# Performance work log

Hardware: AMD Instinct MI355X
Metric: run time of the kernel (lower is better)

## Reference

```python
import jax, jax.numpy as jnp
import numpy as np

B, L, DIM = 1, 2048, 4096
H, KV, HD = 32, 8, 128
REP = H // KV
SCALE = HD ** -0.5
ROPE_BASE = 10000.0


def rope_traditional(x, offset=0):
    # x: [B, H, L, D] ; traditional RoPE rotates interleaved pairs (x[2i], x[2i+1])
    D = x.shape[-1]
    Lx = x.shape[2]
    pos = jnp.arange(offset, offset + Lx, dtype=jnp.float32)            # [L]
    inv_freq = ROPE_BASE ** (-jnp.arange(0, D, 2, dtype=jnp.float32) / D)  # [D/2]
    ang = pos[:, None] * inv_freq[None, :]                               # [L, D/2]
    c, s = jnp.cos(ang), jnp.sin(ang)
    x1 = x[..., 0::2]
    x2 = x[..., 1::2]
    r1 = x1 * c - x2 * s
    r2 = x1 * s + x2 * c
    return jnp.stack([r1, r2], axis=-1).reshape(x.shape).astype(x.dtype)


def setup_inputs() -> dict:
    key = jax.random.key(0)
    k0, k1, k2, k3, k4 = jax.random.split(key, 5)
    x = jax.random.normal(k0, (B, L, DIM), dtype=jnp.float32)
    wq = jax.random.normal(k1, (DIM, H * HD), dtype=jnp.float32) * 0.02
    wk = jax.random.normal(k2, (DIM, KV * HD), dtype=jnp.float32) * 0.02
    wv = jax.random.normal(k3, (DIM, KV * HD), dtype=jnp.float32) * 0.02
    wo = jax.random.normal(k4, (H * HD, DIM), dtype=jnp.float32) * 0.02
    # additive causal mask (prefill)
    causal = jnp.tril(jnp.ones((L, L), dtype=bool))
    mask = jnp.where(causal, 0.0, -1e9).astype(jnp.float32)
    return {"x": x, "wq": wq, "wk": wk, "wv": wv, "wo": wo, "mask": mask}


def reference(x, wq, wk, wv, wo, mask):
    Bx, Lx, _ = x.shape
    q = (x @ wq).reshape(Bx, Lx, H, HD).transpose(0, 2, 1, 3)   # [B,H,L,hd]
    k = (x @ wk).reshape(Bx, Lx, KV, HD).transpose(0, 2, 1, 3)  # [B,KV,L,hd]
    v = (x @ wv).reshape(Bx, Lx, KV, HD).transpose(0, 2, 1, 3)
    # GQA head repeat (each kv head repeated REP times contiguously)
    k = jnp.repeat(k, REP, axis=1)  # [B,H,L,hd]
    v = jnp.repeat(v, REP, axis=1)
    # RoPE applied after repeat (cache=None branch), offset 0
    q = rope_traditional(q)
    k = rope_traditional(k)
    scores = jnp.einsum("bhld,bhmd->bhlm", q * SCALE, k) + mask  # [B,H,L,L]
    probs = jax.nn.softmax(scores.astype(jnp.float32), axis=-1).astype(scores.dtype)
    out = jnp.einsum("bhlm,bhmd->bhld", probs, v)
    out = out.transpose(0, 2, 1, 3).reshape(Bx, Lx, H * HD)
    return out @ wo, k, v
```

## Files before the change

### kernel.cpp

```cpp
#include <hip/hip_runtime.h>
#include <hip/hip_bf16.h>
#include <math.h>


#define L_SEQ 2048
#define DIM   4096
#define NH    32
#define NKV   8
#define HD    128
#define SCALE 0.08838834764831845f

typedef __bf16 bf16x8 __attribute__((ext_vector_type(8)));
typedef __bf16 bf16x4 __attribute__((ext_vector_type(4)));
typedef __bf16 bf16x2 __attribute__((ext_vector_type(2)));
typedef float  f32x4  __attribute__((ext_vector_type(4)));

__device__ __forceinline__ void gld16(const void* g, void* l) {
  __builtin_amdgcn_global_load_lds(
      (const __attribute__((address_space(1))) void*)g,
      (__attribute__((address_space(3))) void*)l, 16, 0, 0);
}

__global__ void cast_bf16_kernel(const float* __restrict__ in,
                                 __bf16* __restrict__ out, long n4) {
  long i = blockIdx.x * (long)blockDim.x + threadIdx.x;
  if (i >= n4) return;
  float4 f = reinterpret_cast<const float4*>(in)[i];
  bf16x4 o;
  o[0] = (__bf16)f.x; o[1] = (__bf16)f.y; o[2] = (__bf16)f.z; o[3] = (__bf16)f.w;
  reinterpret_cast<bf16x4*>(out)[i] = o;
}

__global__ void tcast_kernel(const float* __restrict__ in0, __bf16* __restrict__ out0,
                             const float* __restrict__ in1, __bf16* __restrict__ out1,
                             int K, int N) {
  __shared__ float tile[32][33];
  const float* in  = blockIdx.z ? in1  : in0;
  __bf16*     out  = blockIdx.z ? out1 : out0;
  int n0 = blockIdx.x * 32, k0 = blockIdx.y * 32;
  int tx = threadIdx.x & 31, ty = threadIdx.x >> 5;
#pragma unroll
  for (int i = 0; i < 4; ++i)
    tile[ty + i * 8][tx] = in[(long)(k0 + ty + i * 8) * N + n0 + tx];
  __syncthreads();
#pragma unroll
  for (int i = 0; i < 4; ++i)
    out[(long)(n0 + ty + i * 8) * K + k0 + tx] = (__bf16)tile[tx][ty + i * 8];
}

#define GBM 128
#define GBN 256
#define ABYTES  (GBM * 64 * 2)
#define BBYTES  (GBN * 64 * 2)
#define BUFBYTES (ABYTES + BBYTES)

__global__ __launch_bounds__(512, 2) void gemm256(
    const __bf16* __restrict__ A, const __bf16* __restrict__ B0,
    const __bf16* __restrict__ B1, void* __restrict__ C0, void* __restrict__ C1,
    int M, int N, int K, int mode) {
  __shared__ char lds[3 * BUFBYTES] __attribute__((aligned(16)));
  const __bf16* Bt = blockIdx.z ? B1 : B0;
  void* C = blockIdx.z ? C1 : C0;

  const int nwg = gridDim.x * gridDim.y;
  const int bid = blockIdx.y * gridDim.x + blockIdx.x;
  const int swz = (bid & 7) * (nwg >> 3) + (bid >> 3);
  const int n0 = (swz % gridDim.x) * GBN;
  const int m0 = (swz / gridDim.x) * GBM;

  const int t = threadIdx.x, wave = t >> 6, lane = t & 63;
  const int quad = lane >> 4, l16 = lane & 15;
  const int wm = (wave >> 2) * 64, wn = (wave & 3) * 64;

  const int srow = t >> 3;
  const int scol = ((t & 7) ^ (srow & 7)) * 8;
  const __bf16* pa = A  + (long)(m0 + srow) * K + scol;
  const __bf16* pb = Bt + (long)(n0 + srow) * K + scol;
  const long K64 = (long)64 * K;
  const int ldsA = wave * 1024;
  const int ldsB = ABYTES + wave * 1024;

  int aoff[2][4], boff[2][4];
#pragma unroll
  for (int ks = 0; ks < 2; ++ks) {
    const int sw = ((ks * 4 + quad) ^ (l16 & 7)) * 16;
#pragma unroll
    for (int i = 0; i < 4; ++i) {
      aoff[ks][i] = (wm + i * 16 + l16) * 128 + sw;
      boff[ks][i] = ABYTES + (wn + i * 16 + l16) * 128 + sw;
    }
  }

  f32x4 acc[4][4] = {};
  const int nt = K >> 6;

  {
    char* bb = lds;
#pragma unroll
    for (int pt = 0; pt < 2; ++pt) {
      gld16(pa,           bb + ldsA);
      gld16(pa + K64,     bb + ldsA + 8192);
      gld16(pb,           bb + ldsB);
      gld16(pb + K64,     bb + ldsB + 8192);
      gld16(pb + 2 * K64, bb + ldsB + 16384);
      gld16(pb + 3 * K64, bb + ldsB + 24576);
      pa += 64; pb += 64;
      bb += BUFBYTES;
    }
  }

  char* cb = lds;
  char* sb = lds + 2 * BUFBYTES;

#pragma unroll 1
  for (int kt = 0; kt < nt - 1; ++kt) {
    asm volatile("s_waitcnt vmcnt(6)" ::: "memory");
    __builtin_amdgcn_s_barrier();
    bf16x8 af[4], bfr[4];
#pragma unroll
    for (int i = 0; i < 4; ++i) {
      af[i]  = *(const bf16x8*)(cb + aoff[0][i]);
      bfr[i] = *(const bf16x8*)(cb + boff[0][i]);
    }
    if (kt + 2 < nt) {
      gld16(pa,           sb + ldsA);
      gld16(pa + K64,     sb + ldsA + 8192);
      gld16(pb,           sb + ldsB);
      gld16(pb + K64,     sb + ldsB + 8192);
      gld16(pb + 2 * K64, sb + ldsB + 16384);
      gld16(pb + 3 * K64, sb + ldsB + 24576);
      pa += 64; pb += 64;
    }
    __builtin_amdgcn_s_setprio(1);
#pragma unroll
    for (int tm = 0; tm < 4; ++tm)
#pragma unroll
      for (int tn = 0; tn < 4; ++tn)
        acc[tm][tn] = __builtin_amdgcn_mfma_f32_16x16x32_bf16(
            af[tm], bfr[tn], acc[tm][tn], 0, 0, 0);
    __builtin_amdgcn_s_setprio(0);
#pragma unroll
    for (int i = 0; i < 4; ++i) {
      af[i]  = *(const bf16x8*)(cb + aoff[1][i]);
      bfr[i] = *(const bf16x8*)(cb + boff[1][i]);
    }
    __builtin_amdgcn_s_setprio(1);
#pragma unroll
    for (int tm = 0; tm < 4; ++tm)
#pragma unroll
      for (int tn = 0; tn < 4; ++tn)
        acc[tm][tn] = __builtin_amdgcn_mfma_f32_16x16x32_bf16(
            af[tm], bfr[tn], acc[tm][tn], 0, 0, 0);
    __builtin_amdgcn_s_setprio(0);
    cb += BUFBYTES; if (cb == lds + 3 * BUFBYTES) cb = lds;
    sb += BUFBYTES; if (sb == lds + 3 * BUFBYTES) sb = lds;
  }

  asm volatile("s_waitcnt vmcnt(0)" ::: "memory");
  __builtin_amdgcn_s_barrier();
  {
    bf16x8 af[4], bfr[4];
#pragma unroll
    for (int ks = 0; ks < 2; ++ks) {
#pragma unroll
      for (int i = 0; i < 4; ++i) {
        af[i]  = *(const bf16x8*)(cb + aoff[ks][i]);
        bfr[i] = *(const bf16x8*)(cb + boff[ks][i]);
      }
      __builtin_amdgcn_s_setprio(1);
#pragma unroll
      for (int tm = 0; tm < 4; ++tm)
#pragma unroll
        for (int tn = 0; tn < 4; ++tn)
          acc[tm][tn] = __builtin_amdgcn_mfma_f32_16x16x32_bf16(
              af[tm], bfr[tn], acc[tm][tn], 0, 0, 0);
      __builtin_amdgcn_s_setprio(0);
    }
  }

#pragma unroll
  for (int tm = 0; tm < 4; ++tm)
#pragma unroll
    for (int tn = 0; tn < 4; ++tn)
#pragma unroll
      for (int r = 0; r < 4; ++r) {
        int row = m0 + wm + tm * 16 + quad * 4 + r;
        int col = n0 + wn + tn * 16 + l16;
        float v = acc[tm][tn][r];
        if (mode == 0) {
          ((float*)C)[(long)row * N + col] = v;
        } else {
          long idx = ((long)(col >> 7) * L_SEQ + row) * HD + (col & 127);
          ((__bf16*)C)[idx] = (__bf16)v;
        }
      }
}

#define NLOG2_10K 13.287712379549449f

__global__ void rope_q_kernel(__bf16* __restrict__ q ) {
  int idx = blockIdx.x * blockDim.x + threadIdx.x;
  int i = idx & 63, l = (idx >> 6) & 2047, h = idx >> 17;
  if (h >= NH) return;
  long base = ((long)h * L_SEQ + l) * HD + 2 * i;
  bf16x2 x12 = *(bf16x2*)(q + base);
  float x1 = (float)x12[0], x2 = (float)x12[1];
  float inv = exp2f((float)i * (-NLOG2_10K / 64.0f));
  float s, c; __sincosf((float)l * inv, &s, &c);
  bf16x2 o; o[0] = (__bf16)(x1 * c - x2 * s); o[1] = (__bf16)(x1 * s + x2 * c);
  *(bf16x2*)(q + base) = o;
}

__global__ void ropekv_kernel(__bf16* __restrict__ kb ,
                              const __bf16* __restrict__ vb,
                              float* __restrict__ kout ,
                              float* __restrict__ vout) {
  int idx = blockIdx.x * blockDim.x + threadIdx.x;
  int i = idx & 63, l = (idx >> 6) & 2047, kv = idx >> 17;
  if (kv >= NKV) return;
  long base = ((long)kv * L_SEQ + l) * HD + 2 * i;
  bf16x2 x12 = *(bf16x2*)(kb + base);
  float x1 = (float)x12[0], x2 = (float)x12[1];
  float inv = exp2f((float)i * (-NLOG2_10K / 64.0f));
  float s, c; __sincosf((float)l * inv, &s, &c);
  float r1 = x1 * c - x2 * s, r2 = x1 * s + x2 * c;
  bf16x2 o; o[0] = (__bf16)r1; o[1] = (__bf16)r2;
  *(bf16x2*)(kb + base) = o;
  float2 kf; kf.x = r1; kf.y = r2;
  bf16x2 vv = *(const bf16x2*)(vb + base);
  float2 vf; vf.x = (float)vv[0]; vf.y = (float)vv[1];
  long off = (long)(kv * 4) * L_SEQ * HD + (long)l * HD + 2 * i;
#pragma unroll
  for (int rr = 0; rr < 4; ++rr) {
    *(float2*)(kout + off) = kf;
    *(float2*)(vout + off) = vf;
    off += (long)L_SEQ * HD;
  }
}

__global__ void vtrans_kernel(const __bf16* __restrict__ Vh, __bf16* __restrict__ Vt) {
  __shared__ __bf16 tile[64 * 65];
  int kv = blockIdx.z, lb = blockIdx.x * 64, db = blockIdx.y * 64;
  int t = threadIdx.x;
#pragma unroll
  for (int it = 0; it < 2; ++it) {
    int c = it * 256 + t, r = c >> 3, pc = c & 7;
    bf16x8 v = *(const bf16x8*)(Vh + ((long)kv * L_SEQ + lb + r) * HD + db + pc * 8);
#pragma unroll
    for (int e = 0; e < 8; ++e) tile[r * 65 + pc * 8 + e] = v[e];
  }
  __syncthreads();
#pragma unroll
  for (int it = 0; it < 2; ++it) {
    int c = it * 256 + t, r = c >> 3, pc = c & 7;
    bf16x8 v;
#pragma unroll
    for (int e = 0; e < 8; ++e) v[e] = tile[(pc * 8 + e) * 65 + r];
    *(bf16x8*)(Vt + ((long)kv * HD + db + r) * L_SEQ + lb + pc * 8) = v;
  }
}

#define PSP 72
#define DTHR 8.0f

__global__ __launch_bounds__(256, 1) void attn4_kernel(
    const __bf16* __restrict__ Q, const __bf16* __restrict__ K,
    const __bf16* __restrict__ Vt, __bf16* __restrict__ O ) {
  __shared__ __bf16 Ks[2][64 * 128]  __attribute__((aligned(16)));
  __shared__ __bf16 Vts[2][128 * 64] __attribute__((aligned(16)));
  __shared__ __bf16 Ps[128 * PSP]    __attribute__((aligned(16)));

  const int b = blockIdx.x;
  const int kvg = b & 7;
  const int h   = kvg * 4 + ((b >> 3) & 3);
  const int qt  = 15 - (b >> 5);
  const int t = threadIdx.x, wave = t >> 6, lane = t & 63;
  const int quad = lane >> 4, l16 = lane & 15;
  const int mw = wave * 32;
  const __bf16* Kh = K  + (long)kvg * L_SEQ * HD;
  const __bf16* Vh = Vt + (long)kvg * HD * L_SEQ;
  const float SL2 = SCALE * 1.44269504f;

  int kr[4], kk[4], vr[4], vk[4];
#pragma unroll
  for (int it = 0; it < 4; ++it) {
    int c = it * 256 + t;
    kr[it] = c >> 4; kk[it] = ((c & 15) ^ (kr[it] & 7)) * 8;
    vr[it] = c >> 3; vk[it] = ((c & 7)  ^ (vr[it] & 7)) * 8;
  }

  const int nchunk = 2 * qt + 2;
  const int jdiag  = 2 * qt;

  int mq[2]; mq[0] = qt * 128 + mw + l16; mq[1] = mq[0] + 16;

  bf16x8 bq[2][4];
#pragma unroll
  for (int g = 0; g < 2; ++g) {
    const __bf16* qrow = Q + ((long)h * L_SEQ + mq[g]) * HD + quad * 8;
#pragma unroll
    for (int d = 0; d < 4; ++d) bq[g][d] = *(const bf16x8*)(qrow + d * 32);
  }

  f32x4 o_acc[2][8] = {};
  float m_run[2] = {-1e30f, -1e30f}, l_run[2] = {0.f, 0.f};

#pragma unroll
  for (int it = 0; it < 4; ++it) {
    gld16(Kh + (long)kr[it] * HD + kk[it],
          (char*)Ks[0] + (size_t)(it * 256 + wave * 64) * 16);
    gld16(Vh + (long)vr[it] * L_SEQ + vk[it],
          (char*)Vts[0] + (size_t)(it * 256 + wave * 64) * 16);
  }

#pragma unroll 1
  for (int j = 0; j < nchunk; ++j) {
    const int cur = j & 1;
    __syncthreads();
    if (j + 1 < nchunk) {
      const int nxt = cur ^ 1;
#pragma unroll
      for (int it = 0; it < 4; ++it) {
        gld16(Kh + (long)((j + 1) * 64 + kr[it]) * HD + kk[it],
              (char*)Ks[nxt] + (size_t)(it * 256 + wave * 64) * 16);
        gld16(Vh + (long)vr[it] * L_SEQ + (j + 1) * 64 + vk[it],
              (char*)Vts[nxt] + (size_t)(it * 256 + wave * 64) * 16);
      }
    }

    f32x4 s[2][4] = {};
#pragma unroll
    for (int dsi = 0; dsi < 4; ++dsi)
#pragma unroll
      for (int tn = 0; tn < 4; ++tn) {
        bf16x8 ak = *(const bf16x8*)((char*)Ks[cur] + (tn * 16 + l16) * 256 +
                                     (((dsi * 4 + quad) ^ (l16 & 7)) * 16));
        s[0][tn] = __builtin_amdgcn_mfma_f32_16x16x32_bf16(ak, bq[0][dsi], s[0][tn], 0, 0, 0);
        s[1][tn] = __builtin_amdgcn_mfma_f32_16x16x32_bf16(ak, bq[1][dsi], s[1][tn], 0, 0, 0);
      }

#pragma unroll
    for (int g = 0; g < 2; ++g) {
#pragma unroll
      for (int tn = 0; tn < 4; ++tn)
#pragma unroll
        for (int r = 0; r < 4; ++r) {
          float v = s[g][tn][r] * SL2;
          if (j >= jdiag && (j * 64 + tn * 16 + quad * 4 + r) > mq[g]) v = -3.0e38f;
          s[g][tn][r] = v;
        }
      float mx = -3.0e38f;
#pragma unroll
      for (int tn = 0; tn < 4; ++tn)
#pragma unroll
        for (int r = 0; r < 4; ++r) mx = fmaxf(mx, s[g][tn][r]);
      mx = fmaxf(mx, __shfl_xor(mx, 16, 64));
      mx = fmaxf(mx, __shfl_xor(mx, 32, 64));

      const bool defer = __all(mx - m_run[g] <= DTHR);
      const float mnew = defer ? m_run[g] : fmaxf(m_run[g], mx);

      float rs = 0.f;
#pragma unroll
      for (int tn = 0; tn < 4; ++tn)
#pragma unroll
        for (int r = 0; r < 4; ++r) {
          float pe = exp2f(s[g][tn][r] - mnew);
          s[g][tn][r] = pe; rs += pe;
        }
      rs += __shfl_xor(rs, 16, 64);
      rs += __shfl_xor(rs, 32, 64);

      if (defer) {
        l_run[g] += rs;
      } else {
        float alpha = exp2f(m_run[g] - mnew);
#pragma unroll
        for (int td = 0; td < 8; ++td)
#pragma unroll
          for (int r = 0; r < 4; ++r) o_acc[g][td][r] *= alpha;
        l_run[g] = l_run[g] * alpha + rs;
        m_run[g] = mnew;
      }

#pragma unroll
      for (int tn = 0; tn < 4; ++tn) {
        bf16x4 pv;
#pragma unroll
        for (int r = 0; r < 4; ++r) pv[r] = (__bf16)s[g][tn][r];
        *(bf16x4*)(&Ps[(mw + g * 16 + l16) * PSP + tn * 16 + quad * 4]) = pv;
      }
    }

#pragma unroll
    for (int ks = 0; ks < 2; ++ks) {
      bf16x8 bp0 = *(const bf16x8*)(&Ps[(mw + l16) * PSP + ks * 32 + quad * 8]);
      bf16x8 bp1 = *(const bf16x8*)(&Ps[(mw + 16 + l16) * PSP + ks * 32 + quad * 8]);
#pragma unroll
      for (int td = 0; td < 8; ++td) {
        bf16x8 av = *(const bf16x8*)((char*)Vts[cur] + (td * 16 + l16) * 128 +
                                     (((ks * 4 + quad) ^ (l16 & 7)) * 16));
        o_acc[0][td] = __builtin_amdgcn_mfma_f32_16x16x32_bf16(av, bp0, o_acc[0][td], 0, 0, 0);
        o_acc[1][td] = __builtin_amdgcn_mfma_f32_16x16x32_bf16(av, bp1, o_acc[1][td], 0, 0, 0);
      }
    }
  }

#pragma unroll
  for (int g = 0; g < 2; ++g) {
    float inv_l = 1.0f / l_run[g];
#pragma unroll
    for (int td = 0; td < 8; ++td) {
      bf16x4 ov;
#pragma unroll
      for (int r = 0; r < 4; ++r) ov[r] = (__bf16)(o_acc[g][td][r] * inv_l);
      *(bf16x4*)(O + (long)mq[g] * DIM + h * HD + td * 16 + quad * 4) = ov;
    }
  }
}

extern "C" void kernel_launch(void* const* d_in, const int* in_sizes, int n_in,
                              void* d_out, int out_size, void* d_ws, size_t ws_size,
                              hipStream_t stream) {
  const float* x  = (const float*)d_in[0];
  const float* wq = (const float*)d_in[1];
  const float* wk = (const float*)d_in[2];
  const float* wv = (const float*)d_in[3];
  const float* wo = (const float*)d_in[4];

  float* out   = (float*)d_out;
  float* k_out = out + (long)L_SEQ * DIM;
  float* v_out = k_out + (long)NH * L_SEQ * HD;

  char* ws = (char*)d_ws;
  __bf16* Xb  = (__bf16*)ws; ws += (long)L_SEQ * DIM * 2;
  __bf16* Wqt = (__bf16*)ws; ws += (long)DIM * DIM * 2;
  __bf16* Wkt = (__bf16*)ws; ws += (long)DIM * (NKV * HD) * 2;
  __bf16* Wvt = (__bf16*)ws; ws += (long)DIM * (NKV * HD) * 2;
  __bf16* Wot = (__bf16*)ws; ws += (long)DIM * DIM * 2;
  __bf16* Qh  = (__bf16*)ws; ws += (long)NH * L_SEQ * HD * 2;
  __bf16* Kh  = (__bf16*)ws; ws += (long)NKV * L_SEQ * HD * 2;
  __bf16* Vh  = (__bf16*)ws; ws += (long)NKV * L_SEQ * HD * 2;
  __bf16* Vt  = (__bf16*)ws; ws += (long)NKV * HD * L_SEQ * 2;
  __bf16* Ob  = (__bf16*)ws; ws += (long)L_SEQ * DIM * 2;

  tcast_kernel<<<dim3(DIM / 32, DIM / 32, 1), 256, 0, stream>>>(wq, Wqt, wq, Wqt, DIM, DIM);
  tcast_kernel<<<dim3((NKV * HD) / 32, DIM / 32, 2), 256, 0, stream>>>(wk, Wkt, wv, Wvt, DIM, NKV * HD);
  tcast_kernel<<<dim3(DIM / 32, DIM / 32, 1), 256, 0, stream>>>(wo, Wot, wo, Wot, DIM, DIM);
  {
    long n = (long)L_SEQ * DIM;
    cast_bf16_kernel<<<dim3(n / 1024), 256, 0, stream>>>(x, Xb, n / 4);
  }
  gemm256<<<dim3(DIM / 256, L_SEQ / 128, 1), 512, 0, stream>>>(
      Xb, Wqt, Wqt, Qh, Qh, L_SEQ, DIM, DIM, 2);
  gemm256<<<dim3((NKV * HD) / 256, L_SEQ / 128, 2), 512, 0, stream>>>(
      Xb, Wkt, Wvt, Kh, Vh, L_SEQ, NKV * HD, DIM, 2);
  rope_q_kernel<<<dim3((NH * L_SEQ * 64) / 256), 256, 0, stream>>>(Qh);
  ropekv_kernel<<<dim3((NKV * L_SEQ * 64) / 256), 256, 0, stream>>>(Kh, Vh, k_out, v_out);
  vtrans_kernel<<<dim3(L_SEQ / 64, HD / 64, NKV), 256, 0, stream>>>(Vh, Vt);
  attn4_kernel<<<dim3(512), 256, 0, stream>>>(Qh, Kh, Vt, Ob);
  gemm256<<<dim3(DIM / 256, L_SEQ / 128, 1), 512, 0, stream>>>(
      Ob, Wot, Wot, out, out, L_SEQ, DIM, DIM, 0);
}
```

Baseline: 572.1 us.

## Template GEMM tile width, raise attention occupancy, swizzle P buffer, rebalance tiles

Templates the GEMM on output tile width and launches the K/V projection with 128-wide tiles to double its block count and fill more CUs. The attention kernel now asks for two blocks per CU, replaces the padded P staging buffer with an XOR-swizzled unpadded layout that cuts LDS use, and reorders query tiles so heavy and light causal tiles interleave. The risks are register pressure from the tighter launch bound and lower per-block reuse in the narrower GEMM.

```diff
diff --git a/kernel.cpp b/kernel.cpp
--- a/kernel.cpp
+++ b/kernel.cpp
@@ -48,29 +48,28 @@
     out[(long)(n0 + ty + i * 8) * K + k0 + tx] = (__bf16)tile[tx][ty + i * 8];
 }
 
-#define GBM 128
-#define GBN 256
-#define ABYTES  (GBM * 64 * 2)
-#define BBYTES  (GBN * 64 * 2)
-#define BUFBYTES (ABYTES + BBYTES)
-
-__global__ __launch_bounds__(512, 2) void gemm256(
+template<int TN>
+__global__ __launch_bounds__(512, 2) void gemm_t(
     const __bf16* __restrict__ A, const __bf16* __restrict__ B0,
     const __bf16* __restrict__ B1, void* __restrict__ C0, void* __restrict__ C1,
     int M, int N, int K, int mode) {
-  __shared__ char lds[3 * BUFBYTES] __attribute__((aligned(16)));
+  constexpr int TNF = TN / 64;
+  constexpr int ABY = 128 * 64 * 2;
+  constexpr int BBY = TN * 64 * 2;
+  constexpr int BUF = ABY + BBY;
+  __shared__ char lds[3 * BUF] __attribute__((aligned(16)));
   const __bf16* Bt = blockIdx.z ? B1 : B0;
   void* C = blockIdx.z ? C1 : C0;
 
   const int nwg = gridDim.x * gridDim.y;
   const int bid = blockIdx.y * gridDim.x + blockIdx.x;
   const int swz = (bid & 7) * (nwg >> 3) + (bid >> 3);
-  const int n0 = (swz % gridDim.x) * GBN;
-  const int m0 = (swz / gridDim.x) * GBM;
+  const int n0 = (swz % gridDim.x) * TN;
+  const int m0 = (swz / gridDim.x) * 128;
 
   const int t = threadIdx.x, wave = t >> 6, lane = t & 63;
   const int quad = lane >> 4, l16 = lane & 15;
-  const int wm = (wave >> 2) * 64, wn = (wave & 3) * 64;
+  const int wm = (wave >> 2) * 64, wn = (wave & 3) * (TN / 4);
 
   const int srow = t >> 3;
   const int scol = ((t & 7) ^ (srow & 7)) * 8;
@@ -78,100 +77,95 @@
   const __bf16* pb = Bt + (long)(n0 + srow) * K + scol;
   const long K64 = (long)64 * K;
   const int ldsA = wave * 1024;
-  const int ldsB = ABYTES + wave * 1024;
-
-  int aoff[2][4], boff[2][4];
+  const int ldsB = ABY + wave * 1024;
+
+  int aoff[2][4], boff[2][TN / 64];
 #pragma unroll
   for (int ks = 0; ks < 2; ++ks) {
     const int sw = ((ks * 4 + quad) ^ (l16 & 7)) * 16;
 #pragma unroll
-    for (int i = 0; i < 4; ++i) {
+    for (int i = 0; i < 4; ++i)
       aoff[ks][i] = (wm + i * 16 + l16) * 128 + sw;
-      boff[ks][i] = ABYTES + (wn + i * 16 + l16) * 128 + sw;
-    }
-  }
-
-  f32x4 acc[4][4] = {};
+#pragma unroll
+    for (int i = 0; i < TN / 64; ++i)
+      boff[ks][i] = ABY + (wn + i * 16 + l16) * 128 + sw;
+  }
+
+  f32x4 acc[4][TN / 64] = {};
   const int nt = K >> 6;
 
   {
     char* bb = lds;
 #pragma unroll
     for (int pt = 0; pt < 2; ++pt) {
-      gld16(pa,           bb + ldsA);
-      gld16(pa + K64,     bb + ldsA + 8192);
-      gld16(pb,           bb + ldsB);
-      gld16(pb + K64,     bb + ldsB + 8192);
-      gld16(pb + 2 * K64, bb + ldsB + 16384);
-      gld16(pb + 3 * K64, bb + ldsB + 24576);
+#pragma unroll
+      for (int r = 0; r < 2; ++r) gld16(pa + r * K64, bb + ldsA + r * 8192);
+#pragma unroll
+      for (int r = 0; r < TN / 64; ++r) gld16(pb + r * K64, bb + ldsB + r * 8192);
       pa += 64; pb += 64;
-      bb += BUFBYTES;
+      bb += BUF;
     }
   }
 
   char* cb = lds;
-  char* sb = lds + 2 * BUFBYTES;
+  char* sb = lds + 2 * BUF;
 
 #pragma unroll 1
   for (int kt = 0; kt < nt - 1; ++kt) {
-    asm volatile("s_waitcnt vmcnt(6)" ::: "memory");
+    if constexpr (TN == 256) asm volatile("s_waitcnt vmcnt(6)" ::: "memory");
+    else                     asm volatile("s_waitcnt vmcnt(4)" ::: "memory");
     __builtin_amdgcn_s_barrier();
-    bf16x8 af[4], bfr[4];
-#pragma unroll
-    for (int i = 0; i < 4; ++i) {
-      af[i]  = *(const bf16x8*)(cb + aoff[0][i]);
-      bfr[i] = *(const bf16x8*)(cb + boff[0][i]);
-    }
+    bf16x8 af[4], bfr[TN / 64];
+#pragma unroll
+    for (int i = 0; i < 4; ++i) af[i] = *(const bf16x8*)(cb + aoff[0][i]);
+#pragma unroll
+    for (int i = 0; i < TN / 64; ++i) bfr[i] = *(const bf16x8*)(cb + boff[0][i]);
     if (kt + 2 < nt) {
-      gld16(pa,           sb + ldsA);
-      gld16(pa + K64,     sb + ldsA + 8192);
-      gld16(pb,           sb + ldsB);
-      gld16(pb + K64,     sb + ldsB + 8192);
-      gld16(pb + 2 * K64, sb + ldsB + 16384);
-      gld16(pb + 3 * K64, sb + ldsB + 24576);
+#pragma unroll
+      for (int r = 0; r < 2; ++r) gld16(pa + r * K64, sb + ldsA + r * 8192);
+#pragma unroll
+      for (int r = 0; r < TN / 64; ++r) gld16(pb + r * K64, sb + ldsB + r * 8192);
       pa += 64; pb += 64;
     }
     __builtin_amdgcn_s_setprio(1);
 #pragma unroll
     for (int tm = 0; tm < 4; ++tm)
 #pragma unroll
-      for (int tn = 0; tn < 4; ++tn)
+      for (int tn = 0; tn < TN / 64; ++tn)
         acc[tm][tn] = __builtin_amdgcn_mfma_f32_16x16x32_bf16(
             af[tm], bfr[tn], acc[tm][tn], 0, 0, 0);
     __builtin_amdgcn_s_setprio(0);
 #pragma unroll
-    for (int i = 0; i < 4; ++i) {
-      af[i]  = *(const bf16x8*)(cb + aoff[1][i]);
-      bfr[i] = *(const bf16x8*)(cb + boff[1][i]);
-    }
+    for (int i = 0; i < 4; ++i) af[i] = *(const bf16x8*)(cb + aoff[1][i]);
+#pragma unroll
+    for (int i = 0; i < TN / 64; ++i) bfr[i] = *(const bf16x8*)(cb + boff[1][i]);
     __builtin_amdgcn_s_setprio(1);
 #pragma unroll
     for (int tm = 0; tm < 4; ++tm)
 #pragma unroll
-      for (int tn = 0; tn < 4; ++tn)
+      for (int tn = 0; tn < TN / 64; ++tn)
         acc[tm][tn] = __builtin_amdgcn_mfma_f32_16x16x32_bf16(
             af[tm], bfr[tn], acc[tm][tn], 0, 0, 0);
     __builtin_amdgcn_s_setprio(0);
-    cb += BUFBYTES; if (cb == lds + 3 * BUFBYTES) cb = lds;
-    sb += BUFBYTES; if (sb == lds + 3 * BUFBYTES) sb = lds;
+    cb += BUF; if (cb == lds + 3 * BUF) cb = lds;
+    sb += BUF; if (sb == lds + 3 * BUF) sb = lds;
   }
 
   asm volatile("s_waitcnt vmcnt(0)" ::: "memory");
   __builtin_amdgcn_s_barrier();
   {
-    bf16x8 af[4], bfr[4];
+    bf16x8 af[4], bfr[TN / 64];
 #pragma unroll
     for (int ks = 0; ks < 2; ++ks) {
 #pragma unroll
-      for (int i = 0; i < 4; ++i) {
-        af[i]  = *(const bf16x8*)(cb + aoff[ks][i]);
-        bfr[i] = *(const bf16x8*)(cb + boff[ks][i]);
-      }
+      for (int i = 0; i < 4; ++i) af[i] = *(const bf16x8*)(cb + aoff[ks][i]);
+#pragma unroll
+      for (int i = 0; i < TN / 64; ++i) bfr[i] = *(const bf16x8*)(cb + boff[ks][i]);
       __builtin_amdgcn_s_setprio(1);
 #pragma unroll
       for (int tm = 0; tm < 4; ++tm)
 #pragma unroll
-        for (int tn = 0; tn < 4; ++tn)
+        for (int tn = 0; tn < TN / 64; ++tn)
           acc[tm][tn] = __builtin_amdgcn_mfma_f32_16x16x32_bf16(
               af[tm], bfr[tn], acc[tm][tn], 0, 0, 0);
       __builtin_amdgcn_s_setprio(0);
@@ -181,7 +175,7 @@
 #pragma unroll
   for (int tm = 0; tm < 4; ++tm)
 #pragma unroll
-    for (int tn = 0; tn < 4; ++tn)
+    for (int tn = 0; tn < TN / 64; ++tn)
 #pragma unroll
       for (int r = 0; r < 4; ++r) {
         int row = m0 + wm + tm * 16 + quad * 4 + r;
@@ -260,20 +254,20 @@
   }
 }
 
-#define PSP 72
 #define DTHR 8.0f
 
-__global__ __launch_bounds__(256, 1) void attn4_kernel(
+__global__ __launch_bounds__(256, 2) void attn4_kernel(
     const __bf16* __restrict__ Q, const __bf16* __restrict__ K,
     const __bf16* __restrict__ Vt, __bf16* __restrict__ O ) {
   __shared__ __bf16 Ks[2][64 * 128]  __attribute__((aligned(16)));
   __shared__ __bf16 Vts[2][128 * 64] __attribute__((aligned(16)));
-  __shared__ __bf16 Ps[128 * PSP]    __attribute__((aligned(16)));
+  __shared__ __bf16 Ps[128 * 64]     __attribute__((aligned(16)));
 
   const int b = blockIdx.x;
   const int kvg = b & 7;
   const int h   = kvg * 4 + ((b >> 3) & 3);
-  const int qt  = 15 - (b >> 5);
+  const int i16 = b >> 5;
+  const int qt  = (i16 < 8) ? (15 - i16) : (i16 - 8);
   const int t = threadIdx.x, wave = t >> 6, lane = t & 63;
   const int quad = lane >> 4, l16 = lane & 15;
   const int mw = wave * 32;
@@ -388,14 +382,17 @@
         bf16x4 pv;
 #pragma unroll
         for (int r = 0; r < 4; ++r) pv[r] = (__bf16)s[g][tn][r];
-        *(bf16x4*)(&Ps[(mw + g * 16 + l16) * PSP + tn * 16 + quad * 4]) = pv;
+        *(bf16x4*)((char*)Ps + (mw + g * 16 + l16) * 128 +
+                   ((tn * 32 + quad * 8) ^ ((l16 & 7) << 4))) = pv;
       }
     }
 
 #pragma unroll
     for (int ks = 0; ks < 2; ++ks) {
-      bf16x8 bp0 = *(const bf16x8*)(&Ps[(mw + l16) * PSP + ks * 32 + quad * 8]);
-      bf16x8 bp1 = *(const bf16x8*)(&Ps[(mw + 16 + l16) * PSP + ks * 32 + quad * 8]);
+      bf16x8 bp0 = *(const bf16x8*)((char*)Ps + (mw + l16) * 128 +
+                                    ((ks * 64 + quad * 16) ^ ((l16 & 7) << 4)));
+      bf16x8 bp1 = *(const bf16x8*)((char*)Ps + (mw + 16 + l16) * 128 +
+                                    ((ks * 64 + quad * 16) ^ ((l16 & 7) << 4)));
 #pragma unroll
       for (int td = 0; td < 8; ++td) {
         bf16x8 av = *(const bf16x8*)((char*)Vts[cur] + (td * 16 + l16) * 128 +
@@ -451,14 +448,14 @@
     long n = (long)L_SEQ * DIM;
     cast_bf16_kernel<<<dim3(n / 1024), 256, 0, stream>>>(x, Xb, n / 4);
   }
-  gemm256<<<dim3(DIM / 256, L_SEQ / 128, 1), 512, 0, stream>>>(
+  gemm_t<256><<<dim3(DIM / 256, L_SEQ / 128, 1), 512, 0, stream>>>(
       Xb, Wqt, Wqt, Qh, Qh, L_SEQ, DIM, DIM, 2);
-  gemm256<<<dim3((NKV * HD) / 256, L_SEQ / 128, 2), 512, 0, stream>>>(
+  gemm_t<128><<<dim3((NKV * HD) / 128, L_SEQ / 128, 2), 512, 0, stream>>>(
       Xb, Wkt, Wvt, Kh, Vh, L_SEQ, NKV * HD, DIM, 2);
   rope_q_kernel<<<dim3((NH * L_SEQ * 64) / 256), 256, 0, stream>>>(Qh);
   ropekv_kernel<<<dim3((NKV * L_SEQ * 64) / 256), 256, 0, stream>>>(Kh, Vh, k_out, v_out);
   vtrans_kernel<<<dim3(L_SEQ / 64, HD / 64, NKV), 256, 0, stream>>>(Vh, Vt);
   attn4_kernel<<<dim3(512), 256, 0, stream>>>(Qh, Kh, Vt, Ob);
-  gemm256<<<dim3(DIM / 256, L_SEQ / 128, 1), 512, 0, stream>>>(
+  gemm_t<256><<<dim3(DIM / 256, L_SEQ / 128, 1), 512, 0, stream>>>(
       Ob, Wot, Wot, out, out, L_SEQ, DIM, DIM, 0);
 }
```

Result: faster. 546.1 us (-4.6%).
